# Kernel tuning notes

Hardware: AMD Instinct MI355X
Metric: run time of the kernel (lower is better)

The kernel has to match this reference:

```python
import jax, jax.numpy as jnp
import numpy as np
import math

D_MODEL = 1024
N_HEADS = 16
D_K = D_MODEL // N_HEADS
B, T = 4, 2048


def setup_inputs() -> dict:
    key = jax.random.key(0)
    ks = jax.random.split(key, 6)
    scale = 1.0 / math.sqrt(D_MODEL)
    x = jax.random.normal(ks[0], (B, T, D_MODEL), dtype=jnp.float32)
    Wq_w = jax.random.normal(ks[1], (D_MODEL, D_MODEL), dtype=jnp.float32) * scale
    Wk_w = jax.random.normal(ks[2], (D_MODEL, D_MODEL), dtype=jnp.float32) * scale
    Wv_w = jax.random.normal(ks[3], (D_MODEL, D_MODEL), dtype=jnp.float32) * scale
    Wo_w = jax.random.normal(ks[4], (D_MODEL, D_MODEL), dtype=jnp.float32) * scale
    zb = jnp.zeros((D_MODEL,), dtype=jnp.float32)
    # causal mask [1,1,T,T]: 1 where attention allowed (lower triangular)
    mask = jnp.tril(jnp.ones((T, T), dtype=jnp.int32))[None, None, :, :]
    return {
        "x": x, "mask": mask,
        "Wq_w": Wq_w, "Wq_b": zb, "Wk_w": Wk_w, "Wk_b": zb,
        "Wv_w": Wv_w, "Wv_b": zb, "Wo_w": Wo_w, "Wo_b": zb,
    }


def reference(x, mask, Wq_w, Wq_b, Wk_w, Wk_b, Wv_w, Wv_b, Wo_w, Wo_b):
    Bs, Ts, C = x.shape
    # nn.Linear: y = x @ W.T + b
    q = (x @ Wq_w.T + Wq_b).reshape(Bs, Ts, N_HEADS, D_K).transpose(0, 2, 1, 3)
    k = (x @ Wk_w.T + Wk_b).reshape(Bs, Ts, N_HEADS, D_K).transpose(0, 2, 1, 3)
    v = (x @ Wv_w.T + Wv_b).reshape(Bs, Ts, N_HEADS, D_K).transpose(0, 2, 1, 3)
    # scores: [B, H, T, T]
    scores = jnp.einsum('bhqd,bhkd->bhqk', q, k) / math.sqrt(D_K)
    scores = jnp.where(mask == 0, -jnp.inf, scores)
    probs = jax.nn.softmax(scores, axis=-1)
    # dropout=0 (eval) -> identity
    out = jnp.einsum('bhqk,bhkd->bhqd', probs, v)
    out = out.transpose(0, 2, 1, 3).reshape(Bs, Ts, C)
    return out @ Wo_w.T + Wo_b
```

## Files before the change

kernel.cpp:

```cpp
#include <hip/hip_runtime.h>


#define AS1 __attribute__((address_space(1)))
#define AS3 __attribute__((address_space(3)))

typedef __attribute__((ext_vector_type(8))) short bf16x8;
typedef __attribute__((ext_vector_type(4))) float f32x4;

constexpr int T_SEQ = 2048;
constexpr int DMODEL = 1024;
constexpr int NH = 16;
constexpr int DK = 64;

#if __has_builtin(__builtin_amdgcn_exp2f)
#define EXP2(x) __builtin_amdgcn_exp2f(x)
#else
#define EXP2(x) exp2f(x)
#endif
#if __has_builtin(__builtin_amdgcn_rcpf)
#define RCP(x) __builtin_amdgcn_rcpf(x)
#else
#define RCP(x) (1.0f / (x))
#endif

__device__ __forceinline__ unsigned short f2bf(float f) {
  union { float f; unsigned u; } v; v.f = f;
  return (unsigned short)((v.u + 0x7fffu + ((v.u >> 16) & 1u)) >> 16);
}

__global__ void cast_f32_bf16(const float4* __restrict__ in, ushort4* __restrict__ out, int n4) {
  int i = blockIdx.x * blockDim.x + threadIdx.x;
  if (i < n4) {
    float4 f = in[i];
    ushort4 o;
    o.x = f2bf(f.x); o.y = f2bf(f.y); o.z = f2bf(f.z); o.w = f2bf(f.w);
    out[i] = o;
  }
}

__global__ void cast_w4(const float4* __restrict__ a, const float4* __restrict__ b,
                        const float4* __restrict__ c, const float4* __restrict__ d,
                        ushort4* __restrict__ oa, ushort4* __restrict__ ob,
                        ushort4* __restrict__ oc, ushort4* __restrict__ od, int n4) {
  int i = blockIdx.x * blockDim.x + threadIdx.x;
  if (i >= n4) return;
  const float4* src = (blockIdx.y == 0) ? a : (blockIdx.y == 1) ? b : (blockIdx.y == 2) ? c : d;
  ushort4* dst = (blockIdx.y == 0) ? oa : (blockIdx.y == 1) ? ob : (blockIdx.y == 2) ? oc : od;
  float4 f = src[i];
  ushort4 o;
  o.x = f2bf(f.x); o.y = f2bf(f.y); o.z = f2bf(f.z); o.w = f2bf(f.w);
  dst[i] = o;
}

__device__ __forceinline__ void gload_lds16(const ushort* g, ushort* l) {
  __builtin_amdgcn_global_load_lds((AS1 void*)g, (AS3 void*)l, 16, 0, 0);
}

__device__ __forceinline__ void gemm_mainloop(
    const ushort* __restrict__ A, const ushort* __restrict__ Bw,
    ushort* As, ushort* Bs, int m0, int n0, f32x4 acc[4][4])
{
  const int t = threadIdx.x;
  const int lane = t & 63;
  const int wave = t >> 6;
  const int wm = (wave & 1) * 64;
  const int wn = (wave >> 1) * 64;
  const int lr = lane & 15;
  const int quad = lane >> 4;

  for (int k0 = 0; k0 < DMODEL; k0 += 32) {
    __syncthreads();
#pragma unroll
    for (int i = 0; i < 2; ++i) {
      const int c0 = i * 256 + wave * 64;
      const int c = c0 + lane;
      gload_lds16(A + (size_t)(m0 + (c >> 2)) * DMODEL + k0 + (c & 3) * 8, As + c0 * 8);
      gload_lds16(Bw + (size_t)(n0 + (c >> 2)) * DMODEL + k0 + (c & 3) * 8, Bs + c0 * 8);
    }
    __syncthreads();
    bf16x8 af[4], bfr[4];
#pragma unroll
    for (int mt = 0; mt < 4; ++mt)
      af[mt] = *(const bf16x8*)(As + (wm + mt * 16 + lr) * 32 + quad * 8);
#pragma unroll
    for (int nt = 0; nt < 4; ++nt)
      bfr[nt] = *(const bf16x8*)(Bs + (wn + nt * 16 + lr) * 32 + quad * 8);
#pragma unroll
    for (int mt = 0; mt < 4; ++mt)
#pragma unroll
      for (int nt = 0; nt < 4; ++nt)
        acc[mt][nt] = __builtin_amdgcn_mfma_f32_16x16x32_bf16(af[mt], bfr[nt], acc[mt][nt], 0, 0, 0);
  }
}

__global__ __launch_bounds__(256, 2) void gemm_qkv(
    const ushort* __restrict__ xb,
    const ushort* __restrict__ wq, const ushort* __restrict__ wk, const ushort* __restrict__ wv,
    const float* __restrict__ bq, const float* __restrict__ bk, const float* __restrict__ bv,
    ushort* __restrict__ Qb, ushort* __restrict__ Kb, ushort* __restrict__ Vt)
{
  __shared__ __align__(16) ushort As[128 * 32];
  __shared__ __align__(16) ushort Bs[128 * 32];
  __shared__ __align__(16) ushort ep[4][2560];
  const int n0 = blockIdx.x * 128;
  const int m0 = blockIdx.y * 128;
  const int z = blockIdx.z;
  const ushort* W = (z == 0) ? wq : (z == 1) ? wk : wv;
  const float* bias = (z == 0) ? bq : (z == 1) ? bk : bv;
  f32x4 acc[4][4] = {};
  gemm_mainloop(xb, W, As, Bs, m0, n0, acc);

  const int lane = threadIdx.x & 63;
  const int wave = threadIdx.x >> 6;
  const int wm = (wave & 1) * 64, wn = (wave >> 1) * 64;
  const int lr = lane & 15, quad = lane >> 4;
  const float scale = (z == 0) ? 0.1803368801111204f : 1.0f;
  ushort* dstQK = (z == 0) ? Qb : Kb;
  ushort* myep = ep[wave];
  const int hgrp = (n0 + wn) >> 6;
  const int mbase = m0 + wm;
  const int bidx = mbase >> 11;

  float bn4[4];
#pragma unroll
  for (int nt = 0; nt < 4; ++nt) bn4[nt] = bias[n0 + wn + nt * 16 + lr];

#pragma unroll
  for (int ph = 0; ph < 2; ++ph) {
    if (z < 2) {
#pragma unroll
      for (int mi = 0; mi < 2; ++mi) {
        const int mt = ph * 2 + mi;
#pragma unroll
        for (int nt = 0; nt < 4; ++nt)
#pragma unroll
          for (int r = 0; r < 4; ++r)
            myep[(mi * 16 + quad * 4 + r) * 72 + nt * 16 + lr] =
                f2bf((acc[mt][nt][r] + bn4[nt]) * scale);
      }
      asm volatile("s_waitcnt lgkmcnt(0)" ::: "memory");
#pragma unroll
      for (int p = 0; p < 4; ++p) {
        const int ml = p * 8 + (lane >> 3);
        const int ck = (lane & 7) * 8;
        const int4 v = *(const int4*)(myep + ml * 72 + ck);
        const int tt = (mbase + ph * 32 + ml) & 2047;
        *(int4*)(dstQK + (((size_t)(bidx * NH + hgrp) * T_SEQ + tt) << 6) + ck) = v;
      }
      asm volatile("s_waitcnt lgkmcnt(0)" ::: "memory");
    } else {
#pragma unroll
      for (int mi = 0; mi < 2; ++mi) {
        const int mt = ph * 2 + mi;
#pragma unroll
        for (int nt = 0; nt < 4; ++nt) {
          ushort4 qv;
          qv.x = f2bf(acc[mt][nt][0] + bn4[nt]);
          qv.y = f2bf(acc[mt][nt][1] + bn4[nt]);
          qv.z = f2bf(acc[mt][nt][2] + bn4[nt]);
          qv.w = f2bf(acc[mt][nt][3] + bn4[nt]);
          *(ushort4*)(myep + (nt * 16 + lr) * 40 + mi * 16 + quad * 4) = qv;
        }
      }
      asm volatile("s_waitcnt lgkmcnt(0)" ::: "memory");
#pragma unroll
      for (int p = 0; p < 4; ++p) {
        const int nl = p * 16 + (lane >> 2);
        const int ck = (lane & 3) * 8;
        const int4 v = *(const int4*)(myep + nl * 40 + ck);
        const int tb = (mbase + ph * 32) & 2047;
        *(int4*)(Vt + (((size_t)(bidx * NH + hgrp) * DK + nl) << 11) + tb + ck) = v;
      }
      asm volatile("s_waitcnt lgkmcnt(0)" ::: "memory");
    }
  }
}

__global__ __launch_bounds__(128, 4) void attn_fwd(
    const ushort* __restrict__ Qb, const ushort* __restrict__ Kb,
    const ushort* __restrict__ Vt, ushort* __restrict__ attn)
{
  __shared__ __align__(16) float smf[2][1056];
  __shared__ float psd[2][16];
  const int u = blockIdx.x;
  const int bh = u & 63;
  const int qsub = 63 - (u >> 6);
  const int lane = threadIdx.x & 63;
  const int wv = threadIdx.x >> 6;
  const int lr = lane & 15, quad = lane >> 4;
  const int q0w = qsub * 32;
  const ushort* Qh = Qb + (size_t)bh * T_SEQ * DK;
  const ushort* Kh = Kb + (size_t)bh * T_SEQ * DK;
  const ushort* Vh = Vt + (size_t)bh * DK * T_SEQ;
  ushort* kbuf = (ushort*)smf[wv];

  const int idx0 = (lr + ((lane & 16) ? 32 : 0)) << 2;
  const int idx1 = idx0 + 64;
  const bool hiHalf = (lane & 32) != 0;

  const int srow = lane >> 3;
  const int scol = ((lane & 7) ^ srow) * 8;
  const int c0 = (quad ^ (lr & 7)) * 8;
  const int c1 = c0 ^ 32;

  bf16x8 qf[2][2];
#pragma unroll
  for (int mf = 0; mf < 2; ++mf)
#pragma unroll
    for (int h = 0; h < 2; ++h)
      qf[mf][h] = *(const bf16x8*)(Qh + (size_t)(q0w + mf * 16 + lr) * DK + h * 32 + quad * 8);

  f32x4 o[2][4];
  float ps[2] = {0.f, 0.f};
#pragma unroll
  for (int mf = 0; mf < 2; ++mf)
#pragma unroll
    for (int nt = 0; nt < 4; ++nt) o[mf][nt] = (f32x4){0.f, 0.f, 0.f, 0.f};

  auto stageK = [&](int t) {
    const int kv0 = t * 32;
#pragma unroll
    for (int s = 0; s < 4; ++s)
      gload_lds16(Kh + (size_t)(kv0 + s * 8 + srow) * DK + scol, kbuf + s * 512);
  };

  auto compute = [&](int t) {
    const int kv0 = t * 32;
    const bool masked = (t == qsub);
    bf16x8 vf[4];
#pragma unroll
    for (int nt = 0; nt < 4; ++nt)
      vf[nt] = *(const bf16x8*)(Vh + (size_t)(nt * 16 + lr) * T_SEQ + kv0 + quad * 8);

    unsigned pk[2][2][2];
#pragma unroll
    for (int cc = 0; cc < 2; ++cc) {
      const int kvc = kv0 + cc * 16;
      const bf16x8 kf0 = *(const bf16x8*)(kbuf + (cc * 16 + lr) * 64 + c0);
      const bf16x8 kf1 = *(const bf16x8*)(kbuf + (cc * 16 + lr) * 64 + c1);
#pragma unroll
      for (int mf = 0; mf < 2; ++mf) {
        f32x4 st = (f32x4){0.f, 0.f, 0.f, 0.f};
        st = __builtin_amdgcn_mfma_f32_16x16x32_bf16(kf0, qf[mf][0], st, 0, 0, 0);
        st = __builtin_amdgcn_mfma_f32_16x16x32_bf16(kf1, qf[mf][1], st, 0, 0, 0);
        float p[4];
#pragma unroll
        for (int r = 0; r < 4; ++r) {
          float e = EXP2(st[r]);
          if (masked) {
            const int ki = kvc + quad * 4 + r;
            const int qi = q0w + mf * 16 + lr;
            e = (ki <= qi) ? e : 0.f;
          }
          p[r] = e;
        }
        ps[mf] += (p[0] + p[1]) + (p[2] + p[3]);
        pk[mf][cc][0] = __builtin_amdgcn_perm(__float_as_uint(p[1]), __float_as_uint(p[0]), 0x07060302u);
        pk[mf][cc][1] = __builtin_amdgcn_perm(__float_as_uint(p[3]), __float_as_uint(p[2]), 0x07060302u);
      }
    }
#pragma unroll
    for (int mf = 0; mf < 2; ++mf) {
      int4 pr;
      {
        const int a = __builtin_amdgcn_ds_bpermute(idx0, (int)pk[mf][0][0]);
        const int b = __builtin_amdgcn_ds_bpermute(idx0, (int)pk[mf][1][0]);
        pr.x = hiHalf ? b : a;
      }
      {
        const int a = __builtin_amdgcn_ds_bpermute(idx0, (int)pk[mf][0][1]);
        const int b = __builtin_amdgcn_ds_bpermute(idx0, (int)pk[mf][1][1]);
        pr.y = hiHalf ? b : a;
      }
      {
        const int a = __builtin_amdgcn_ds_bpermute(idx1, (int)pk[mf][0][0]);
        const int b = __builtin_amdgcn_ds_bpermute(idx1, (int)pk[mf][1][0]);
        pr.z = hiHalf ? b : a;
      }
      {
        const int a = __builtin_amdgcn_ds_bpermute(idx1, (int)pk[mf][0][1]);
        const int b = __builtin_amdgcn_ds_bpermute(idx1, (int)pk[mf][1][1]);
        pr.w = hiHalf ? b : a;
      }
      union { int4 i; bf16x8 v; } pa;
      pa.i = pr;
#pragma unroll
      for (int nt = 0; nt < 4; ++nt)
        o[mf][nt] = __builtin_amdgcn_mfma_f32_16x16x32_bf16(pa.v, vf[nt], o[mf][nt], 0, 0, 0);
    }
  };

  {
    int ti = wv;
    if (ti <= qsub) {
      stageK(ti);
      while (true) {
        asm volatile("s_waitcnt vmcnt(0)" ::: "memory");
        compute(ti);
        const int tn = ti + 2;
        if (tn > qsub) break;
        asm volatile("s_waitcnt lgkmcnt(0)" ::: "memory");
        stageK(tn);
        ti = tn;
      }
    }
  }

#pragma unroll
  for (int mf = 0; mf < 2; ++mf) {
    float v = ps[mf];
    v += __shfl_xor(v, 16);
    v += __shfl_xor(v, 32);
    ps[mf] = v;
  }

  f32x4 okeep[4], odump[4];
  float pskeep, psdump;
  if (wv == 0) {
#pragma unroll
    for (int nt = 0; nt < 4; ++nt) { okeep[nt] = o[0][nt]; odump[nt] = o[1][nt]; }
    pskeep = ps[0]; psdump = ps[1];
  } else {
#pragma unroll
    for (int nt = 0; nt < 4; ++nt) { okeep[nt] = o[1][nt]; odump[nt] = o[0][nt]; }
    pskeep = ps[1]; psdump = ps[0];
  }

  float* dumpw = smf[wv];
#pragma unroll
  for (int nt = 0; nt < 4; ++nt)
#pragma unroll
    for (int r = 0; r < 4; ++r)
      dumpw[(quad * 4 + r) * 66 + nt * 16 + lr] = odump[nt][r];
  if (quad == 0) psd[wv][lr] = psdump;
  __syncthreads();

  const float* dumpo = smf[1 - wv];
  const float tot = pskeep + psd[1 - wv][lr];
  const float inv = RCP(tot);
  float oo[4][4];
#pragma unroll
  for (int nt = 0; nt < 4; ++nt)
#pragma unroll
    for (int r = 0; r < 4; ++r)
      oo[nt][r] = okeep[nt][r] + dumpo[(quad * 4 + r) * 66 + nt * 16 + lr];
  __syncthreads();

  ushort* Po = (ushort*)smf;
#pragma unroll
  for (int r = 0; r < 4; ++r) {
    union { int i; float f; } iv;
    iv.i = __builtin_amdgcn_ds_bpermute((quad * 4 + r) << 2, __float_as_int(inv));
#pragma unroll
    for (int nt = 0; nt < 4; ++nt)
      Po[(wv * 16 + quad * 4 + r) * 64 + nt * 16 + lr] = f2bf(oo[nt][r] * iv.f);
  }

  const int b = bh >> 4, h = bh & 15;
#pragma unroll
  for (int it = 0; it < 2; ++it) {
    const int row = wv * 16 + it * 8 + (lane >> 3);
    const int col8 = (lane & 7) * 8;
    const int4 val = *(const int4*)(Po + row * 64 + col8);
    *(int4*)(attn + (size_t)(b * T_SEQ + q0w + row) * DMODEL + h * DK + col8) = val;
  }
}

__global__ __launch_bounds__(256, 2) void gemm_out(
    const ushort* __restrict__ attn, const ushort* __restrict__ wo,
    const float* __restrict__ bo, float* __restrict__ out)
{
  __shared__ __align__(16) ushort As[128 * 32];
  __shared__ __align__(16) ushort Bs[128 * 32];
  const int n0 = blockIdx.x * 128;
  const int m0 = blockIdx.y * 128;
  f32x4 acc[4][4] = {};
  gemm_mainloop(attn, wo, As, Bs, m0, n0, acc);
  const int lane = threadIdx.x & 63, wave = threadIdx.x >> 6;
  const int wm = (wave & 1) * 64, wn = (wave >> 1) * 64;
  const int lr = lane & 15, quad = lane >> 4;
#pragma unroll
  for (int mt = 0; mt < 4; ++mt)
#pragma unroll
    for (int nt = 0; nt < 4; ++nt) {
      const int n = n0 + wn + nt * 16 + lr;
      const float bn = bo[n];
#pragma unroll
      for (int r = 0; r < 4; ++r) {
        const int m = m0 + wm + mt * 16 + quad * 4 + r;
        out[(size_t)m * DMODEL + n] = acc[mt][nt][r] + bn;
      }
    }
}

extern "C" void kernel_launch(void* const* d_in, const int* in_sizes, int n_in,
                              void* d_out, int out_size, void* d_ws, size_t ws_size,
                              hipStream_t stream) {
  const float* x  = (const float*)d_in[0];
  const float* Wq = (const float*)d_in[2];
  const float* bq = (const float*)d_in[3];
  const float* Wk = (const float*)d_in[4];
  const float* bk = (const float*)d_in[5];
  const float* Wv = (const float*)d_in[6];
  const float* bv = (const float*)d_in[7];
  const float* Wo = (const float*)d_in[8];
  const float* bo = (const float*)d_in[9];
  float* out = (float*)d_out;

  const size_t MD = (size_t)8192 * 1024;
  const size_t WD = (size_t)1024 * 1024;
  ushort* ws  = (ushort*)d_ws;
  ushort* xb  = ws;
  ushort* wqb = xb + MD;
  ushort* wkb = wqb + WD;
  ushort* wvb = wkb + WD;
  ushort* wob = wvb + WD;
  ushort* Qb  = wob + WD;
  ushort* Kb  = Qb + MD;
  ushort* Vt  = Kb + MD;
  ushort* att = Vt + MD;

  cast_f32_bf16<<<8192, 256, 0, stream>>>((const float4*)x, (ushort4*)xb, (int)(MD / 4));
  cast_w4<<<dim3(1024, 4), 256, 0, stream>>>(
      (const float4*)Wq, (const float4*)Wk, (const float4*)Wv, (const float4*)Wo,
      (ushort4*)wqb, (ushort4*)wkb, (ushort4*)wvb, (ushort4*)wob, (int)(WD / 4));

  gemm_qkv<<<dim3(8, 64, 3), 256, 0, stream>>>(xb, wqb, wkb, wvb, bq, bk, bv, Qb, Kb, Vt);
  attn_fwd<<<4096, 128, 0, stream>>>(Qb, Kb, Vt, att);
  gemm_out<<<dim3(8, 64), 256, 0, stream>>>(att, wob, bo, out);
}
```

Measured before the change: 300.9 us.

## Split attention KV loop across four waves with two-stage reduction

The attention kernel now launches 256 threads (four waves) per 32-query block instead of two. Each wave strides over KV tiles by four, which shortens the serial KV loop per wave. Partial outputs and row sums are combined in two steps through shared memory: pairs are merged first, then waves 2-3 hand theirs to waves 0-1 for normalisation and output. This adds extra shared-memory traffic and barriers, doubles LDS per block, and may reduce how many blocks fit on a CU.

```diff
diff --git a/kernel.cpp b/kernel.cpp
--- a/kernel.cpp
+++ b/kernel.cpp
@@ -176,23 +176,23 @@
   }
 }
 
-__global__ __launch_bounds__(128, 4) void attn_fwd(
+__global__ __launch_bounds__(256, 4) void attn_fwd(
     const ushort* __restrict__ Qb, const ushort* __restrict__ Kb,
     const ushort* __restrict__ Vt, ushort* __restrict__ attn)
 {
-  __shared__ __align__(16) float smf[2][1056];
-  __shared__ float psd[2][16];
+  __shared__ __align__(16) float smf[4][1056];
+  __shared__ float psd[4][16];
   const int u = blockIdx.x;
   const int bh = u & 63;
   const int qsub = 63 - (u >> 6);
   const int lane = threadIdx.x & 63;
-  const int wv = threadIdx.x >> 6;
+  const int wave = threadIdx.x >> 6;
   const int lr = lane & 15, quad = lane >> 4;
   const int q0w = qsub * 32;
   const ushort* Qh = Qb + (size_t)bh * T_SEQ * DK;
   const ushort* Kh = Kb + (size_t)bh * T_SEQ * DK;
   const ushort* Vh = Vt + (size_t)bh * DK * T_SEQ;
-  ushort* kbuf = (ushort*)smf[wv];
+  ushort* kbuf = (ushort*)smf[wave];
 
   const int idx0 = (lr + ((lane & 16) ? 32 : 0)) << 2;
   const int idx1 = idx0 + 64;
@@ -291,13 +291,13 @@
   };
 
   {
-    int ti = wv;
+    int ti = wave;
     if (ti <= qsub) {
       stageK(ti);
       while (true) {
         asm volatile("s_waitcnt vmcnt(0)" ::: "memory");
         compute(ti);
-        const int tn = ti + 2;
+        const int tn = ti + 4;
         if (tn > qsub) break;
         asm volatile("s_waitcnt lgkmcnt(0)" ::: "memory");
         stageK(tn);
@@ -316,7 +316,7 @@
 
   f32x4 okeep[4], odump[4];
   float pskeep, psdump;
-  if (wv == 0) {
+  if ((wave & 1) == 0) {
 #pragma unroll
     for (int nt = 0; nt < 4; ++nt) { okeep[nt] = o[0][nt]; odump[nt] = o[1][nt]; }
     pskeep = ps[0]; psdump = ps[1];
@@ -326,41 +326,58 @@
     pskeep = ps[1]; psdump = ps[0];
   }
 
-  float* dumpw = smf[wv];
+  float* dumpw = smf[wave];
 #pragma unroll
   for (int nt = 0; nt < 4; ++nt)
 #pragma unroll
     for (int r = 0; r < 4; ++r)
       dumpw[(quad * 4 + r) * 66 + nt * 16 + lr] = odump[nt][r];
-  if (quad == 0) psd[wv][lr] = psdump;
+  if (quad == 0) psd[wave][lr] = psdump;
   __syncthreads();
 
-  const float* dumpo = smf[1 - wv];
-  const float tot = pskeep + psd[1 - wv][lr];
-  const float inv = RCP(tot);
-  float oo[4][4];
-#pragma unroll
-  for (int nt = 0; nt < 4; ++nt)
-#pragma unroll
-    for (int r = 0; r < 4; ++r)
-      oo[nt][r] = okeep[nt][r] + dumpo[(quad * 4 + r) * 66 + nt * 16 + lr];
+  {
+    const float* dumpo = smf[wave ^ 1];
+    pskeep += psd[wave ^ 1][lr];
+#pragma unroll
+    for (int nt = 0; nt < 4; ++nt)
+#pragma unroll
+      for (int r = 0; r < 4; ++r)
+        okeep[nt][r] += dumpo[(quad * 4 + r) * 66 + nt * 16 + lr];
+  }
   __syncthreads();
 
-  ushort* Po = (ushort*)smf;
-#pragma unroll
-  for (int r = 0; r < 4; ++r) {
-    union { int i; float f; } iv;
-    iv.i = __builtin_amdgcn_ds_bpermute((quad * 4 + r) << 2, __float_as_int(inv));
+  if (wave >= 2) {
 #pragma unroll
     for (int nt = 0; nt < 4; ++nt)
-      Po[(wv * 16 + quad * 4 + r) * 64 + nt * 16 + lr] = f2bf(oo[nt][r] * iv.f);
-  }
+#pragma unroll
+      for (int r = 0; r < 4; ++r)
+        dumpw[(quad * 4 + r) * 66 + nt * 16 + lr] = okeep[nt][r];
+    if (quad == 0) psd[wave][lr] = pskeep;
+  }
+  __syncthreads();
+
+  ushort* Po = (ushort*)smf[0];
+  if (wave < 2) {
+    const float* dumpo = smf[wave ^ 2];
+    const float tot = pskeep + psd[wave ^ 2][lr];
+    const float inv = RCP(tot);
+#pragma unroll
+    for (int r = 0; r < 4; ++r) {
+      union { int i; float f; } iv;
+      iv.i = __builtin_amdgcn_ds_bpermute((quad * 4 + r) << 2, __float_as_int(inv));
+#pragma unroll
+      for (int nt = 0; nt < 4; ++nt) {
+        const float vsum = okeep[nt][r] + dumpo[(quad * 4 + r) * 66 + nt * 16 + lr];
+        Po[(wave * 16 + quad * 4 + r) * 64 + nt * 16 + lr] = f2bf(vsum * iv.f);
+      }
+    }
+  }
+  __syncthreads();
 
   const int b = bh >> 4, h = bh & 15;
-#pragma unroll
-  for (int it = 0; it < 2; ++it) {
-    const int row = wv * 16 + it * 8 + (lane >> 3);
-    const int col8 = (lane & 7) * 8;
+  {
+    const int row = threadIdx.x >> 3;
+    const int col8 = (threadIdx.x & 7) * 8;
     const int4 val = *(const int4*)(Po + row * 64 + col8);
     *(int4*)(attn + (size_t)(b * T_SEQ + q0w + row) * DMODEL + h * DK + col8) = val;
   }
@@ -426,6 +443,6 @@
       (ushort4*)wqb, (ushort4*)wkb, (ushort4*)wvb, (ushort4*)wob, (int)(WD / 4));
 
   gemm_qkv<<<dim3(8, 64, 3), 256, 0, stream>>>(xb, wqb, wkb, wvb, bq, bk, bv, Qb, Kb, Vt);
-  attn_fwd<<<4096, 128, 0, stream>>>(Qb, Kb, Vt, att);
+  attn_fwd<<<4096, 256, 0, stream>>>(Qb, Kb, Vt, att);
   gemm_out<<<dim3(8, 64), 256, 0, stream>>>(att, wob, bo, out);
 }
```

Result: slower. 307.9 us (+2.3%).
